# Kernel tuning notes

Hardware: AMD Instinct MI355X
Metric: run time of the kernel (lower is better)

Reference implementation:

```python
import jax, jax.numpy as jnp
import numpy as np

N_NODES = 50000
N_EDGES = 1600000
NODE_DIM = 64
HIDDEN_DIM = 128
EDGE_DIM = 32


def _linear_params(key, fan_in, fan_out, bias=True):
    k1, k2 = jax.random.split(key)
    bound = 1.0 / np.sqrt(fan_in)
    W = jax.random.uniform(k1, (fan_in, fan_out), minval=-bound, maxval=bound, dtype=jnp.float32)
    if bias:
        b = jax.random.uniform(k2, (fan_out,), minval=-bound, maxval=bound, dtype=jnp.float32)
        return W, b
    return W, None


def setup_inputs() -> dict:
    key = jax.random.key(0)
    ks = jax.random.split(key, 12)
    h = jax.random.normal(ks[0], (N_NODES, NODE_DIM), dtype=jnp.float32)
    x = jax.random.normal(ks[1], (N_NODES, 3), dtype=jnp.float32) * 10.0
    edge_index = jax.random.randint(ks[2], (2, N_EDGES), 0, N_NODES, dtype=jnp.int32).astype(jnp.int64)
    edge_dist = jax.random.uniform(ks[3], (N_EDGES,), dtype=jnp.float32) * 10.0

    msg_in = 2 * NODE_DIM + EDGE_DIM
    node_w1, node_b1 = _linear_params(ks[4], msg_in, HIDDEN_DIM)
    node_w2, node_b2 = _linear_params(ks[5], HIDDEN_DIM, NODE_DIM)
    coord_w1, coord_b1 = _linear_params(ks[6], msg_in, HIDDEN_DIM)
    coord_w2, _ = _linear_params(ks[7], HIDDEN_DIM, 1, bias=False)
    edge_w1, edge_b1 = _linear_params(ks[8], 1, EDGE_DIM)
    edge_w2, edge_b2 = _linear_params(ks[9], EDGE_DIM, EDGE_DIM)

    return dict(h=h, x=x, edge_index=edge_index, edge_dist=edge_dist,
                node_w1=node_w1, node_b1=node_b1, node_w2=node_w2, node_b2=node_b2,
                coord_w1=coord_w1, coord_b1=coord_b1, coord_w2=coord_w2,
                edge_w1=edge_w1, edge_b1=edge_b1, edge_w2=edge_w2, edge_b2=edge_b2)


def reference(h, x, edge_index, edge_dist,
              node_w1, node_b1, node_w2, node_b2,
              coord_w1, coord_b1, coord_w2,
              edge_w1, edge_b1, edge_w2, edge_b2):
    src = edge_index[0]
    dst = edge_index[1]

    # edge_mlp: Linear(1, edge_dim) -> SiLU -> Linear(edge_dim, edge_dim)
    edge_attr = jax.nn.silu(edge_dist[:, None] @ edge_w1 + edge_b1) @ edge_w2 + edge_b2

    # per-edge message input: [E, 2*node_dim + edge_dim]
    m_input = jnp.concatenate([h[src], h[dst], edge_attr], axis=-1)

    # node_mlp: Linear -> SiLU -> Linear
    m = jax.nn.silu(m_input @ node_w1 + node_b1) @ node_w2 + node_b2
    h_agg = jnp.zeros_like(h).at[dst].add(m)

    # coord_mlp: Linear -> SiLU -> Linear(hidden, 1, bias=False)
    coord_weight = jax.nn.silu(m_input @ coord_w1 + coord_b1) @ coord_w2  # [E, 1]

    dir_vec = x[src] - x[dst]                               # [E, 3]
    dir_len = jnp.maximum(jnp.linalg.norm(dir_vec, axis=-1, keepdims=True), 1e-8)
    coord_update = coord_weight * (dir_vec / dir_len)
    x_agg = jnp.zeros_like(x).at[dst].add(coord_update)

    return (h + h_agg, x + x_agg)
```

## Files before the change

### kernel.cpp

```cpp
#include <hip/hip_runtime.h>
#include <stdint.h>

#define NN 50000
#define NE 1600000
#define BE 128

typedef __attribute__((ext_vector_type(8))) short short8;
typedef __attribute__((ext_vector_type(4))) float f32x4;

__device__ __forceinline__ unsigned short f2bf(float f) {
    unsigned int u = __float_as_uint(f);
    u += 0x7fff + ((u >> 16) & 1);
    return (unsigned short)(u >> 16);
}

__device__ __forceinline__ float silu_f(float v) {
    return v / (1.0f + __expf(-v));
}

__global__ void prep_kernel(const float* __restrict__ nw1,
                            const float* __restrict__ cw1,
                            const float* __restrict__ nw2,
                            unsigned short* __restrict__ ws) {
    int i = blockIdx.x * 256 + threadIdx.x;
    if (i < 20480) {
        int n = i / 160, k = i % 160;
        ws[i] = f2bf(nw1[k * 128 + n]);
    } else if (i < 40960) {
        int j = i - 20480; int n = j / 160, k = j % 160;
        ws[i] = f2bf(cw1[k * 128 + n]);
    } else if (i < 49152) {
        int j = i - 40960; int o = j / 128, k = j % 128;
        ws[i] = f2bf(nw2[k * 64 + o]);
    }
}

__global__ void init_out(const float4* __restrict__ h4,
                         const float4* __restrict__ x4,
                         float4* __restrict__ out4) {
    int i = blockIdx.x * 256 + threadIdx.x;
    if (i < 800000)       out4[i] = h4[i];
    else if (i < 837500)  out4[i] = x4[i - 800000];
}

#define MIS 168

__global__ __launch_bounds__(256, 2)
void egnn_edge_kernel(const float* __restrict__ h,
                      const float* __restrict__ x,
                      const int* __restrict__ eidx,
                      const float* __restrict__ edist,
                      const float* __restrict__ node_b1,
                      const float* __restrict__ node_b2,
                      const float* __restrict__ coord_b1,
                      const float* __restrict__ coord_w2,
                      const float* __restrict__ ew1,
                      const float* __restrict__ eb1,
                      const float* __restrict__ ew2,
                      const float* __restrict__ eb2,
                      const unsigned short* __restrict__ ws,
                      float* __restrict__ out_h,
                      float* __restrict__ out_x) {
    __shared__ unsigned short mi[BE * MIS];
    __shared__ unsigned short wbuf[64 * MIS];

    const int tid  = threadIdx.x;
    const int w    = tid >> 6;
    const int lane = tid & 63;
    const int ln   = lane & 15;
    const int quad = lane >> 4;
    const int e0   = blockIdx.x * BE;

    {
        const float4* h4 = (const float4*)h;
        const int g = tid >> 4, l16 = tid & 15;
        #pragma unroll
        for (int it = 0; it < 16; ++it) {
            int row = it * 16 + g;
            int e = row & 127;
            int node = (row < 128) ? eidx[e0 + e] : eidx[NE + e0 + e];
            int cbase = (row < 128) ? 0 : 64;
            float4 v = h4[node * 16 + l16];
            unsigned short b[4] = {f2bf(v.x), f2bf(v.y), f2bf(v.z), f2bf(v.w)};
            *(uint2*)&mi[e * MIS + cbase + l16 * 4] = *(uint2*)b;
        }
    }
    {
        int e = tid >> 1, half = tid & 1;
        float d = edist[e0 + e];
        float s[16];
        #pragma unroll
        for (int jj = 0; jj < 16; ++jj) s[jj] = eb2[half * 16 + jj];
        #pragma unroll
        for (int k = 0; k < 32; ++k) {
            float tk = silu_f(d * ew1[k] + eb1[k]);
            const float* r2 = ew2 + k * 32 + half * 16;
            #pragma unroll
            for (int jj = 0; jj < 16; ++jj) s[jj] += tk * r2[jj];
        }
        #pragma unroll
        for (int jj = 0; jj < 16; ++jj)
            mi[e * MIS + 128 + half * 16 + jj] = f2bf(s[jj]);
    }

    f32x4 accN[2][8], accC[2][8];
    const f32x4 zero = {0.f, 0.f, 0.f, 0.f};
    #pragma unroll
    for (int a = 0; a < 2; ++a)
        #pragma unroll
        for (int b = 0; b < 8; ++b) { accN[a][b] = zero; accC[a][b] = zero; }

    const int arow0 = (w * 32 + ln) * MIS;
    const int arow1 = (w * 32 + 16 + ln) * MIS;
    const int koff  = quad * 8;

    #pragma unroll
    for (int pass = 0; pass < 4; ++pass) {
        const int mat = pass >> 1, half = pass & 1;
        const unsigned short* wsrc = ws + mat * 20480 + half * 64 * 160;
        __syncthreads();
        #pragma unroll
        for (int c = 0; c < 5; ++c) {
            int idx = c * 256 + tid;
            int row = idx / 20, col8 = idx % 20;
            *(uint4*)&wbuf[row * MIS + col8 * 8] =
                *(const uint4*)(wsrc + row * 160 + col8 * 8);
        }
        __syncthreads();
        #pragma unroll
        for (int kc = 0; kc < 5; ++kc) {
            short8 a0 = *(const short8*)&mi[arow0 + kc * 32 + koff];
            short8 a1 = *(const short8*)&mi[arow1 + kc * 32 + koff];
            #pragma unroll
            for (int nt = 0; nt < 4; ++nt) {
                short8 b = *(const short8*)&wbuf[(nt * 16 + ln) * MIS + kc * 32 + koff];
                const int nn = half * 4 + nt;
                if (mat == 0) {
                    accN[0][nn] = __builtin_amdgcn_mfma_f32_16x16x32_bf16(a0, b, accN[0][nn], 0, 0, 0);
                    accN[1][nn] = __builtin_amdgcn_mfma_f32_16x16x32_bf16(a1, b, accN[1][nn], 0, 0, 0);
                } else {
                    accC[0][nn] = __builtin_amdgcn_mfma_f32_16x16x32_bf16(a0, b, accC[0][nn], 0, 0, 0);
                    accC[1][nn] = __builtin_amdgcn_mfma_f32_16x16x32_bf16(a1, b, accC[1][nn], 0, 0, 0);
                }
            }
        }
    }

    __syncthreads();
    #pragma unroll
    for (int mt = 0; mt < 2; ++mt) {
        const int rowb = (w * 32 + mt * 16 + quad * 4) * MIS;
        #pragma unroll
        for (int nt = 0; nt < 8; ++nt) {
            int col = nt * 16 + ln;
            float b1v = node_b1[col];
            #pragma unroll
            for (int r = 0; r < 4; ++r)
                mi[rowb + r * MIS + col] = f2bf(silu_f(accN[mt][nt][r] + b1v));
        }
    }
    __syncthreads();

    f32x4 acc2[2][4];
    #pragma unroll
    for (int a = 0; a < 2; ++a)
        #pragma unroll
        for (int b = 0; b < 4; ++b) acc2[a][b] = zero;
    const unsigned short* nw2T = ws + 40960;
    #pragma unroll
    for (int kc = 0; kc < 4; ++kc) {
        short8 a0 = *(const short8*)&mi[arow0 + kc * 32 + koff];
        short8 a1 = *(const short8*)&mi[arow1 + kc * 32 + koff];
        #pragma unroll
        for (int nt = 0; nt < 4; ++nt) {
            short8 b = *(const short8*)(nw2T + (nt * 16 + ln) * 128 + kc * 32 + koff);
            acc2[0][nt] = __builtin_amdgcn_mfma_f32_16x16x32_bf16(a0, b, acc2[0][nt], 0, 0, 0);
            acc2[1][nt] = __builtin_amdgcn_mfma_f32_16x16x32_bf16(a1, b, acc2[1][nt], 0, 0, 0);
        }
    }
    #pragma unroll
    for (int mt = 0; mt < 2; ++mt) {
        #pragma unroll
        for (int r = 0; r < 4; ++r) {
            int lrow = w * 32 + mt * 16 + quad * 4 + r;
            int dn = eidx[NE + e0 + lrow];
            float* outrow = out_h + (size_t)dn * 64;
            #pragma unroll
            for (int nt = 0; nt < 4; ++nt) {
                int col = nt * 16 + ln;
                atomicAdd(outrow + col, acc2[mt][nt][r] + node_b2[col]);
            }
        }
    }

    float cw[2][4];
    #pragma unroll
    for (int mt = 0; mt < 2; ++mt)
        #pragma unroll
        for (int r = 0; r < 4; ++r) cw[mt][r] = 0.f;
    #pragma unroll
    for (int nt = 0; nt < 8; ++nt) {
        int col = nt * 16 + ln;
        float b1v = coord_b1[col];
        float w2v = coord_w2[col];
        #pragma unroll
        for (int mt = 0; mt < 2; ++mt)
            #pragma unroll
            for (int r = 0; r < 4; ++r)
                cw[mt][r] += silu_f(accC[mt][nt][r] + b1v) * w2v;
    }
    #pragma unroll
    for (int off = 1; off < 16; off <<= 1) {
        #pragma unroll
        for (int mt = 0; mt < 2; ++mt)
            #pragma unroll
            for (int r = 0; r < 4; ++r)
                cw[mt][r] += __shfl_xor(cw[mt][r], off, 64);
    }
    if (ln < 8) {
        const int smt = ln >> 2, sr = ln & 3;
        float cwsel = 0.f;
        #pragma unroll
        for (int mt = 0; mt < 2; ++mt)
            #pragma unroll
            for (int r = 0; r < 4; ++r)
                cwsel = (mt == smt && r == sr) ? cw[mt][r] : cwsel;
        int lrow = w * 32 + smt * 16 + quad * 4 + sr;
        int s = eidx[e0 + lrow], dn = eidx[NE + e0 + lrow];
        float dx = x[s * 3]     - x[dn * 3];
        float dy = x[s * 3 + 1] - x[dn * 3 + 1];
        float dz = x[s * 3 + 2] - x[dn * 3 + 2];
        float len = fmaxf(sqrtf(dx * dx + dy * dy + dz * dz), 1e-8f);
        float k = cwsel / len;
        atomicAdd(out_x + dn * 3,     k * dx);
        atomicAdd(out_x + dn * 3 + 1, k * dy);
        atomicAdd(out_x + dn * 3 + 2, k * dz);
    }
}

extern "C" void kernel_launch(void* const* d_in, const int* in_sizes, int n_in,
                              void* d_out, int out_size, void* d_ws, size_t ws_size,
                              hipStream_t stream) {
    const float* h    = (const float*)d_in[0];
    const float* x    = (const float*)d_in[1];
    const int*   eidx = (const int*)d_in[2];
    const float* edist= (const float*)d_in[3];
    const float* nw1  = (const float*)d_in[4];
    const float* nb1  = (const float*)d_in[5];
    const float* nw2  = (const float*)d_in[6];
    const float* nb2  = (const float*)d_in[7];
    const float* cw1  = (const float*)d_in[8];
    const float* cb1  = (const float*)d_in[9];
    const float* cw2  = (const float*)d_in[10];
    const float* ew1  = (const float*)d_in[11];
    const float* eb1  = (const float*)d_in[12];
    const float* ew2  = (const float*)d_in[13];
    const float* eb2  = (const float*)d_in[14];
    float* out = (float*)d_out;
    unsigned short* ws = (unsigned short*)d_ws;

    prep_kernel<<<192, 256, 0, stream>>>(nw1, cw1, nw2, ws);
    init_out<<<3272, 256, 0, stream>>>((const float4*)h, (const float4*)x, (float4*)out);
    egnn_edge_kernel<<<NE / BE, 256, 0, stream>>>(h, x, eidx, edist,
                                                  nb1, nb2, cb1, cw2,
                                                  ew1, eb1, ew2, eb2,
                                                  ws, out, out + 3200000);
}
```

Baseline: 827.3 us.

## Read GEMM weights directly from global memory, drop LDS weight staging, raise occupancy

The kernel no longer stages weight tiles in shared memory with repeated barriers. Each wave now loads B fragments straight from the global bf16 weight buffer, which should mostly hit L2/L1 because every block reads the same weights. A-operand fragments are held in registers for the whole first layer. The coord MLP is computed first and its accumulators are released before the node MLP, which lowers peak register use. Launch bounds rise to 3 blocks per CU to exploit the smaller LDS footprint, trading LDS weight reuse for global/cache loads and possible register pressure or spills.

```diff
diff --git a/kernel.cpp b/kernel.cpp
--- a/kernel.cpp
+++ b/kernel.cpp
@@ -45,7 +45,7 @@
 
 #define MIS 168
 
-__global__ __launch_bounds__(256, 2)
+__global__ __launch_bounds__(256, 3)
 void egnn_edge_kernel(const float* __restrict__ h,
                       const float* __restrict__ x,
                       const int* __restrict__ eidx,
@@ -62,7 +62,6 @@
                       float* __restrict__ out_h,
                       float* __restrict__ out_x) {
     __shared__ unsigned short mi[BE * MIS];
-    __shared__ unsigned short wbuf[64 * MIS];
 
     const int tid  = threadIdx.x;
     const int w    = tid >> 6;
@@ -98,55 +97,121 @@
             #pragma unroll
             for (int jj = 0; jj < 16; ++jj) s[jj] += tk * r2[jj];
         }
-        #pragma unroll
-        for (int jj = 0; jj < 16; ++jj)
-            mi[e * MIS + 128 + half * 16 + jj] = f2bf(s[jj]);
-    }
-
-    f32x4 accN[2][8], accC[2][8];
-    const f32x4 zero = {0.f, 0.f, 0.f, 0.f};
-    #pragma unroll
-    for (int a = 0; a < 2; ++a)
-        #pragma unroll
-        for (int b = 0; b < 8; ++b) { accN[a][b] = zero; accC[a][b] = zero; }
+        unsigned short sb[16];
+        #pragma unroll
+        for (int jj = 0; jj < 16; ++jj) sb[jj] = f2bf(s[jj]);
+        *(uint4*)&mi[e * MIS + 128 + half * 16]     = *(uint4*)&sb[0];
+        *(uint4*)&mi[e * MIS + 128 + half * 16 + 8] = *(uint4*)&sb[8];
+    }
+
+    __syncthreads();
 
     const int arow0 = (w * 32 + ln) * MIS;
     const int arow1 = (w * 32 + 16 + ln) * MIS;
     const int koff  = quad * 8;
-
-    #pragma unroll
-    for (int pass = 0; pass < 4; ++pass) {
-        const int mat = pass >> 1, half = pass & 1;
-        const unsigned short* wsrc = ws + mat * 20480 + half * 64 * 160;
-        __syncthreads();
-        #pragma unroll
-        for (int c = 0; c < 5; ++c) {
-            int idx = c * 256 + tid;
-            int row = idx / 20, col8 = idx % 20;
-            *(uint4*)&wbuf[row * MIS + col8 * 8] =
-                *(const uint4*)(wsrc + row * 160 + col8 * 8);
-        }
-        __syncthreads();
-        #pragma unroll
-        for (int kc = 0; kc < 5; ++kc) {
-            short8 a0 = *(const short8*)&mi[arow0 + kc * 32 + koff];
-            short8 a1 = *(const short8*)&mi[arow1 + kc * 32 + koff];
-            #pragma unroll
-            for (int nt = 0; nt < 4; ++nt) {
-                short8 b = *(const short8*)&wbuf[(nt * 16 + ln) * MIS + kc * 32 + koff];
-                const int nn = half * 4 + nt;
-                if (mat == 0) {
-                    accN[0][nn] = __builtin_amdgcn_mfma_f32_16x16x32_bf16(a0, b, accN[0][nn], 0, 0, 0);
-                    accN[1][nn] = __builtin_amdgcn_mfma_f32_16x16x32_bf16(a1, b, accN[1][nn], 0, 0, 0);
-                } else {
-                    accC[0][nn] = __builtin_amdgcn_mfma_f32_16x16x32_bf16(a0, b, accC[0][nn], 0, 0, 0);
-                    accC[1][nn] = __builtin_amdgcn_mfma_f32_16x16x32_bf16(a1, b, accC[1][nn], 0, 0, 0);
+    const f32x4 zero = {0.f, 0.f, 0.f, 0.f};
+
+    short8 aA[5], aB[5];
+    #pragma unroll
+    for (int kc = 0; kc < 5; ++kc) {
+        aA[kc] = *(const short8*)&mi[arow0 + kc * 32 + koff];
+        aB[kc] = *(const short8*)&mi[arow1 + kc * 32 + koff];
+    }
+
+    const int wvoff = ln * 160 + koff;
+
+    f32x4 accC[2][8];
+    #pragma unroll
+    for (int a = 0; a < 2; ++a)
+        #pragma unroll
+        for (int b = 0; b < 8; ++b) accC[a][b] = zero;
+    {
+        const unsigned short* wsrc = ws + 20480;
+        #pragma unroll
+        for (int half = 0; half < 2; ++half) {
+            #pragma unroll
+            for (int kc = 0; kc < 5; ++kc) {
+                #pragma unroll
+                for (int nt = 0; nt < 4; ++nt) {
+                    short8 b = *(const short8*)(wsrc + half * 10240 + nt * 2560
+                                                + kc * 32 + wvoff);
+                    const int nn = half * 4 + nt;
+                    accC[0][nn] = __builtin_amdgcn_mfma_f32_16x16x32_bf16(aA[kc], b, accC[0][nn], 0, 0, 0);
+                    accC[1][nn] = __builtin_amdgcn_mfma_f32_16x16x32_bf16(aB[kc], b, accC[1][nn], 0, 0, 0);
                 }
             }
         }
     }
 
-    __syncthreads();
+    {
+        float cw[2][4];
+        #pragma unroll
+        for (int mt = 0; mt < 2; ++mt)
+            #pragma unroll
+            for (int r = 0; r < 4; ++r) cw[mt][r] = 0.f;
+        #pragma unroll
+        for (int nt = 0; nt < 8; ++nt) {
+            int col = nt * 16 + ln;
+            float b1v = coord_b1[col];
+            float w2v = coord_w2[col];
+            #pragma unroll
+            for (int mt = 0; mt < 2; ++mt)
+                #pragma unroll
+                for (int r = 0; r < 4; ++r)
+                    cw[mt][r] += silu_f(accC[mt][nt][r] + b1v) * w2v;
+        }
+        #pragma unroll
+        for (int off = 1; off < 16; off <<= 1) {
+            #pragma unroll
+            for (int mt = 0; mt < 2; ++mt)
+                #pragma unroll
+                for (int r = 0; r < 4; ++r)
+                    cw[mt][r] += __shfl_xor(cw[mt][r], off, 64);
+        }
+        if (ln < 8) {
+            const int smt = ln >> 2, sr = ln & 3;
+            float cwsel = 0.f;
+            #pragma unroll
+            for (int mt = 0; mt < 2; ++mt)
+                #pragma unroll
+                for (int r = 0; r < 4; ++r)
+                    cwsel = (mt == smt && r == sr) ? cw[mt][r] : cwsel;
+            int lrow = w * 32 + smt * 16 + quad * 4 + sr;
+            int s = eidx[e0 + lrow], dn = eidx[NE + e0 + lrow];
+            float dx = x[s * 3]     - x[dn * 3];
+            float dy = x[s * 3 + 1] - x[dn * 3 + 1];
+            float dz = x[s * 3 + 2] - x[dn * 3 + 2];
+            float len = fmaxf(sqrtf(dx * dx + dy * dy + dz * dz), 1e-8f);
+            float k = cwsel / len;
+            atomicAdd(out_x + dn * 3,     k * dx);
+            atomicAdd(out_x + dn * 3 + 1, k * dy);
+            atomicAdd(out_x + dn * 3 + 2, k * dz);
+        }
+    }
+
+    f32x4 accN[2][8];
+    #pragma unroll
+    for (int a = 0; a < 2; ++a)
+        #pragma unroll
+        for (int b = 0; b < 8; ++b) accN[a][b] = zero;
+    {
+        const unsigned short* wsrc = ws;
+        #pragma unroll
+        for (int half = 0; half < 2; ++half) {
+            #pragma unroll
+            for (int kc = 0; kc < 5; ++kc) {
+                #pragma unroll
+                for (int nt = 0; nt < 4; ++nt) {
+                    short8 b = *(const short8*)(wsrc + half * 10240 + nt * 2560
+                                                + kc * 32 + wvoff);
+                    const int nn = half * 4 + nt;
+                    accN[0][nn] = __builtin_amdgcn_mfma_f32_16x16x32_bf16(aA[kc], b, accN[0][nn], 0, 0, 0);
+                    accN[1][nn] = __builtin_amdgcn_mfma_f32_16x16x32_bf16(aB[kc], b, accN[1][nn], 0, 0, 0);
+                }
+            }
+        }
+    }
+
     #pragma unroll
     for (int mt = 0; mt < 2; ++mt) {
         const int rowb = (w * 32 + mt * 16 + quad * 4) * MIS;
@@ -159,7 +224,6 @@
                 mi[rowb + r * MIS + col] = f2bf(silu_f(accN[mt][nt][r] + b1v));
         }
     }
-    __syncthreads();
 
     f32x4 acc2[2][4];
     #pragma unroll
@@ -191,50 +255,6 @@
                 atomicAdd(outrow + col, acc2[mt][nt][r] + node_b2[col]);
             }
         }
-    }
-
-    float cw[2][4];
-    #pragma unroll
-    for (int mt = 0; mt < 2; ++mt)
-        #pragma unroll
-        for (int r = 0; r < 4; ++r) cw[mt][r] = 0.f;
-    #pragma unroll
-    for (int nt = 0; nt < 8; ++nt) {
-        int col = nt * 16 + ln;
-        float b1v = coord_b1[col];
-        float w2v = coord_w2[col];
-        #pragma unroll
-        for (int mt = 0; mt < 2; ++mt)
-            #pragma unroll
-            for (int r = 0; r < 4; ++r)
-                cw[mt][r] += silu_f(accC[mt][nt][r] + b1v) * w2v;
-    }
-    #pragma unroll
-    for (int off = 1; off < 16; off <<= 1) {
-        #pragma unroll
-        for (int mt = 0; mt < 2; ++mt)
-            #pragma unroll
-            for (int r = 0; r < 4; ++r)
-                cw[mt][r] += __shfl_xor(cw[mt][r], off, 64);
-    }
-    if (ln < 8) {
-        const int smt = ln >> 2, sr = ln & 3;
-        float cwsel = 0.f;
-        #pragma unroll
-        for (int mt = 0; mt < 2; ++mt)
-            #pragma unroll
-            for (int r = 0; r < 4; ++r)
-                cwsel = (mt == smt && r == sr) ? cw[mt][r] : cwsel;
-        int lrow = w * 32 + smt * 16 + quad * 4 + sr;
-        int s = eidx[e0 + lrow], dn = eidx[NE + e0 + lrow];
-        float dx = x[s * 3]     - x[dn * 3];
-        float dy = x[s * 3 + 1] - x[dn * 3 + 1];
-        float dz = x[s * 3 + 2] - x[dn * 3 + 2];
-        float len = fmaxf(sqrtf(dx * dx + dy * dy + dz * dz), 1e-8f);
-        float k = cwsel / len;
-        atomicAdd(out_x + dn * 3,     k * dx);
-        atomicAdd(out_x + dn * 3 + 1, k * dy);
-        atomicAdd(out_x + dn * 3 + 2, k * dz);
     }
 }
 
```

After: 832.5 us. About the same (+0.6%).
